# Performance work log

Measured on AMD Instinct MI355X. Metric: run time of the kernel, lower is better.

The kernel has to match this reference:

```python
import jax, jax.numpy as jnp
import numpy as np

B, N, C = 8, 16384, 4
NUM_GROUPS = 512   # K for farthest point sampling
GROUP_SIZE = 32    # K after energy-based top-k
UPSCALE_K = 512    # ball-query candidate count
RADIUS = 0.5       # group_radius
CONTEXT = 256      # context_length


def _fps_idx(xyz, lengths, K):
    """Iterative farthest point sampling. xyz: (B,P,3). Returns (B,K) int32 indices.
    Start point is index 0 (random_start_point=False). Assumes lengths >= K."""
    Bn, P, _ = xyz.shape
    valid = jnp.arange(P)[None, :] < lengths[:, None]
    start = jnp.zeros((Bn,), jnp.int32)
    mind0 = jnp.full((Bn, P), jnp.float32(1e10))

    def step(carry, _):
        mind, last = carry
        lastpt = jnp.take_along_axis(xyz, last[:, None, None], axis=1)  # (B,1,3)
        d = jnp.sum((xyz - lastpt) ** 2, axis=-1)                       # (B,P)
        mind = jnp.minimum(mind, d)
        nxt = jnp.argmax(jnp.where(valid, mind, -jnp.inf), axis=1).astype(jnp.int32)
        return (mind, nxt), nxt

    _, rest = jax.lax.scan(step, (mind0, start), None, length=K - 1)  # (K-1,B)
    return jnp.concatenate([start[:, None], rest.T], axis=1)          # (B,K)


def _masked_gather(points, idx):
    """torch masked_gather: -1 indices are replaced with 0 before gathering."""
    idx0 = jnp.maximum(idx, 0)
    if idx.ndim == 3:
        Bn, G, K = idx.shape
        out = jnp.take_along_axis(points, idx0.reshape(Bn, G * K)[:, :, None], axis=1)
        return out.reshape(Bn, G, K, points.shape[-1])
    return jnp.take_along_axis(points, idx0[:, :, None], axis=1)


def _ball_query(centers, xyz, lengths, K, radius):
    """First-K points within radius of each center, in original index order; pad -1."""
    P = xyz.shape[1]
    d2 = jnp.sum((centers[:, :, None, :] - xyz[:, None, :, :]) ** 2, axis=-1)  # (B,G,P)
    valid = (d2 < radius * radius) & (jnp.arange(P)[None, None, :] < lengths[:, None, None])
    # key = -index for valid points, -P for invalid -> top_k gives first valid indices
    key = jnp.where(valid, -jnp.arange(P, dtype=jnp.int32)[None, None, :], jnp.int32(-P))
    vals, pos = jax.lax.top_k(key, K)           # (B,G,K)
    return jnp.where(vals > -P, pos, -1)


def _topk_by_energy(points, idx, K):
    """Keep the K highest-energy (channel 3) points per group; pad -1."""
    Bn, G, Ko = idx.shape
    e = points[..., 3]                                                  # (B,P)
    eb = jnp.broadcast_to(e[:, None, :], (Bn, G, e.shape[1]))
    energies = jnp.take_along_axis(eb, jnp.maximum(idx, 0), axis=2)     # (B,G,Ko)
    energies = jnp.where(idx == -1, -jnp.inf, energies)
    top_e, top_pos = jax.lax.top_k(energies, K)
    top_idx = jnp.take_along_axis(idx, top_pos, axis=2)
    return jnp.where(jnp.isneginf(top_e), -1, top_idx)


def setup_inputs() -> dict:
    key = jax.random.key(0)
    k1, k2 = jax.random.split(key)
    points = jax.random.normal(k1, (B, N, C), dtype=jnp.float32)
    lengths = jax.random.randint(k2, (B,), 3 * N // 4, N + 1, dtype=jnp.int32)
    return {"points": points, "lengths": lengths}


def reference(points, lengths):
    # FPS -> group centers (kept with all C channels, as in masked_gather(points, idx))
    centers_idx = _fps_idx(points[:, :, :3], lengths, NUM_GROUPS)
    group_centers = _masked_gather(points, centers_idx)                 # (B,G,C)
    # Ball query around centers
    idx = _ball_query(group_centers[:, :, :3], points[:, :, :3], lengths, UPSCALE_K, RADIUS)
    # Energy-based reduction to GROUP_SIZE points per group
    idx = _topk_by_energy(points, idx, GROUP_SIZE)                      # (B,G,Ks)
    point_lengths = jnp.sum(idx != -1, axis=2)                          # (B,G)
    # fill_empty_indices: replace -1 with the group's first index
    filled = jnp.where(idx == -1, idx[:, :, :1], idx)
    groups = _masked_gather(points, filled)                             # (B,G,Ks,C)
    point_mask = jnp.arange(GROUP_SIZE)[None, None, :] < point_lengths[:, :CONTEXT, None]
    G = idx.shape[1]
    group_lengths = jnp.sum(jnp.all(idx != -1, axis=2), axis=1)         # (B,)
    embedding_mask = jnp.arange(G)[None, :] < group_lengths[:, None]
    return (groups[:, :CONTEXT], group_centers[:, :CONTEXT],
            embedding_mask[:, :CONTEXT], point_mask)
```

## Files before the change

kernel.cpp:

```cpp
#include <hip/hip_runtime.h>
#include <stdint.h>

#define NB   8
#define NP   16384
#define NG   512
#define GS   32
#define UPK  512
#define CTX  256

#define OFF_CENTERS (NB*CTX*GS*4)
#define OFF_EMB     (OFF_CENTERS + NB*CTX*4)
#define OFF_PMASK   (OFF_EMB + NB*CTX)

typedef unsigned long long u64;
typedef unsigned int u32;

#define SENT32 0xFFFFFFFFu
#define NWK    31

__device__ __forceinline__ u32 fkey(float f) {
  union { float f; u32 u; } v; v.f = f;
  u32 s = v.u;
  return s ^ ((s & 0x80000000u) ? 0xFFFFFFFFu : 0x80000000u);
}

__device__ __forceinline__ float dist2(float ax, float ay, float az,
                                       float bx, float by, float bz) {
  float dx = __fsub_rn(ax, bx);
  float dy = __fsub_rn(ay, by);
  float dz = __fsub_rn(az, bz);
  return __fadd_rn(__fadd_rn(__fmul_rn(dx, dx), __fmul_rn(dy, dy)),
                   __fmul_rn(dz, dz));
}

template<int CTRL, int RM>
__device__ __forceinline__ u64 dpp_max_u64(u64 k) {
  int lo = (int)(u32)k, hi = (int)(u32)(k >> 32);
  int mlo = __builtin_amdgcn_update_dpp(lo, lo, CTRL, RM, 0xf, false);
  int mhi = __builtin_amdgcn_update_dpp(hi, hi, CTRL, RM, 0xf, false);
  u64 o = ((u64)(u32)mhi << 32) | (u32)mlo;
  return o > k ? o : k;
}

__device__ __forceinline__ u64 wave_max_u64(u64 k) {
  k = dpp_max_u64<0x111, 0xf>(k);
  k = dpp_max_u64<0x112, 0xf>(k);
  k = dpp_max_u64<0x114, 0xf>(k);
  k = dpp_max_u64<0x118, 0xf>(k);
  k = dpp_max_u64<0x142, 0xa>(k);
  k = dpp_max_u64<0x143, 0xc>(k);
  return k;
}

__device__ __forceinline__ u64 read_lane_u64(u64 k, int lane) {
  u32 lo = (u32)__builtin_amdgcn_readlane((int)(u32)k, lane);
  u32 hi = (u32)__builtin_amdgcn_readlane((int)(u32)(k >> 32), lane);
  return ((u64)hi << 32) | lo;
}

struct FpsSmem {
  u64 sred[2][8];
};
struct WkSmem {
  u64 masks[256];
  u32 scnt[256];
  u32 spre[256];
  u32 swsum[8];
  float candE[UPK];
  int   candI[UPK];
  int   s_T, s_pl;
  int   s_fin, s_gl;
  int   s_win[GS];
  float4 s_cc;
};
union SmemU { FpsSmem f; WkSmem w; };
struct Smem { SmemU u; char pad[81920]; };

#define FPS_T 512
#define PPT   (NP / FPS_T)

__global__ __launch_bounds__(FPS_T)
__attribute__((amdgpu_waves_per_eu(2, 2)))
void fused_kernel(const float4* __restrict__ pts, const int* __restrict__ lengths,
                  u32* __restrict__ cws, int* __restrict__ group_len,
                  int* __restrict__ wdone, float* __restrict__ out)
{
  __shared__ Smem sm;
  const int blk  = blockIdx.x;
  const int tid  = threadIdx.x;
  const int lane = tid & 63;
  const int wave = tid >> 6;

  if (blk < NB) {
    FpsSmem& F = sm.u.f;
    const int b = blk;
    const float4* p = pts + (size_t)b * NP;
    const int len = lengths[b];
    u32* cb = cws + (size_t)b * NG;
    if (tid == 0)
      __hip_atomic_store(&cb[0], 0u, __ATOMIC_RELAXED, __HIP_MEMORY_SCOPE_AGENT);

    const float4 q0 = p[0];
    float px[PPT], py[PPT], pz[PPT], mind[PPT];
#pragma unroll
    for (int j = 0; j < PPT; j++) {
      int i = tid + j * FPS_T;
      float4 q = p[i];
      if (i >= len) q = q0;
      px[j] = q.x; py[j] = q.y; pz[j] = q.z;
      mind[j] = 1e10f;
    }

    int last = 0;
    for (int it = 1; it < NG; it++) {
      float4 lp = p[last];
      float tmax = -1.0f; int tj = 0;
#pragma unroll
      for (int j = 0; j < PPT; j++) {
        float d = dist2(px[j], py[j], pz[j], lp.x, lp.y, lp.z);
        float m = fminf(mind[j], d);
        mind[j] = m;
        bool c = m > tmax;
        tmax = c ? m : tmax;
        tj   = c ? j : tj;
      }
      int gidx = tid + (tj << 9);
      u64 key = ((u64)__float_as_uint(tmax) << 32) | (u32)(~gidx);
      key = wave_max_u64(key);
      u64 wkey = read_lane_u64(key, 63);
      if (lane == 0) F.sred[it & 1][wave] = wkey;
      __syncthreads();
      u64 k2 = F.sred[it & 1][lane & 7];
      k2 = dpp_max_u64<0x111, 0xf>(k2);
      k2 = dpp_max_u64<0x112, 0xf>(k2);
      k2 = dpp_max_u64<0x114, 0xf>(k2);
      u64 bk = read_lane_u64(k2, 7);
      last = (int)(~(u32)bk) & (NP - 1);
      if (tid == 0)
        __hip_atomic_store(&cb[it], (u32)last, __ATOMIC_RELAXED,
                           __HIP_MEMORY_SCOPE_AGENT);
    }
    return;
  }

  WkSmem& S = sm.u.w;
  const int b  = blk & (NB - 1);
  const int wi = (blk >> 3) - 1;
  const float4* p = pts + (size_t)b * NP;
  const int len = lengths[b];
  u32* cb = cws + (size_t)b * NG;

  for (int g = wi; g < NG; g += NWK) {
    if (tid == 0) {
      u32 ci;
      while ((ci = __hip_atomic_load(&cb[g], __ATOMIC_RELAXED,
                                     __HIP_MEMORY_SCOPE_AGENT)) == SENT32)
        __builtin_amdgcn_s_sleep(8);
      float4 q = p[ci];
      S.s_cc = q;
      if (g < CTX)
        ((float4*)(out + OFF_CENTERS))[b * CTX + g] = q;
    }
    __syncthreads();
    const float cx = S.s_cc.x, cy = S.s_cc.y, cz = S.s_cc.z;

    if (g >= CTX) {
      u32 c = 0;
      for (int step = 0; step < 32; step++) {
        int i = step * 512 + tid;
        bool flag = false;
        if (i < len) {
          float4 q = p[i];
          float d = dist2(cx, cy, cz, q.x, q.y, q.z);
          flag = d < 0.25f;
        }
        c += (u32)__popcll(__ballot(flag));
        if (c >= GS) break;
      }
      if (lane == 0) S.swsum[wave] = c;
      __syncthreads();
      if (tid == 0) {
        u32 total = 0;
#pragma unroll
        for (int w = 0; w < 8; w++) total += S.swsum[w];
        if (total >= GS) atomicAdd(&group_len[b], 1);
      }
      __syncthreads();
      continue;
    }

    for (int step = 0; step < 32; step++) {
      int i = step * 512 + tid;
      bool flag = false;
      if (i < len) {
        float4 q = p[i];
        float d = dist2(cx, cy, cz, q.x, q.y, q.z);
        flag = d < 0.25f;
      }
      u64 m = __ballot(flag);
      if (lane == 0) S.masks[step * 8 + wave] = m;
    }
    __syncthreads();

    u32 cnt = 0, sc = 0;
    if (tid < 256) {
      cnt = (u32)__popcll(S.masks[tid]);
      sc = cnt;
#pragma unroll
      for (int off = 1; off < 64; off <<= 1) {
        u32 o = __shfl_up(sc, (unsigned)off, 64);
        if (lane >= off) sc += o;
      }
      if (lane == 63) S.swsum[wave] = sc;
    }
    __syncthreads();
    const u32 total = S.swsum[0] + S.swsum[1] + S.swsum[2] + S.swsum[3];
    if (tid < 256) {
      u32 woff = 0;
#pragma unroll
      for (int w = 0; w < 4; w++) woff += (w < wave) ? S.swsum[w] : 0u;
      u32 incl = sc + woff;
      S.scnt[tid] = cnt;
      S.spre[tid] = incl;
      if (total > UPK) {
        u32 ex = incl - cnt;
        if (ex <= (UPK - 1) && incl > (UPK - 1)) {
          u32 r = (UPK - 1) - ex;
          u64 m = S.masks[tid];
          for (u32 k = 0; k < r; k++) m &= m - 1;
          S.s_T = tid * 64 + ((int)__ffsll((unsigned long long)m) - 1);
        }
      } else if (tid == 0) S.s_T = NP - 1;
    }
    __syncthreads();
    const int T = S.s_T;

    for (int step = 0; step < 32; step++) {
      int i  = step * 512 + tid;
      int ch = step * 8 + wave;
      u64 m = S.masks[ch];
      if (((m >> lane) & 1ull) && i <= T) {
        u32 pos = ((S.spre[ch] - S.scnt[ch]) +
                   (u32)__popcll(m & ((1ull << lane) - 1ull))) & (UPK - 1);
        S.candE[pos] = ((const float*)p)[i * 4 + 3];
        S.candI[pos] = i;
      }
    }
    __syncthreads();

    const int ncand = (int)(total < UPK ? total : UPK);

    if (wave == 0) {
      u64 k[8];
#pragma unroll
      for (int t = 0; t < 8; t++) {
        int ci = lane + t * 64;
        k[t] = (ci < ncand) ? (((u64)fkey(S.candE[ci]) << 32) | (u32)(~ci)) : 0ull;
      }
      int pl = 0;
      for (int r = 0; r < GS; r++) {
        u64 bm = k[0];
#pragma unroll
        for (int t = 1; t < 8; t++) if (k[t] > bm) bm = k[t];
#pragma unroll
        for (int off = 32; off; off >>= 1) {
          u64 o = __shfl_xor(bm, (unsigned)off, 64);
          if (o > bm) bm = o;
        }
        if (bm == 0) break;
        int pos = (int)(~(u32)bm) & (UPK - 1);
        if (lane == 0) S.s_win[r] = S.candI[pos];
        int ol = pos & 63, ot = pos >> 6;
#pragma unroll
        for (int t = 0; t < 8; t++)
          if (t == ot && lane == ol) k[t] = 0;
        pl = r + 1;
      }
      if (lane == 0) {
        int f0 = (pl > 0) ? S.s_win[0] : 0;
        for (int r = pl; r < GS; r++) S.s_win[r] = f0;
        S.s_pl = pl;
      }
    }
    __syncthreads();

    const int base = b * CTX + g;
    if (tid < GS) {
      int fi = S.s_win[tid] & (NP - 1);
      float4 q = p[fi];
      ((float4*)out)[base * GS + tid] = q;
      out[OFF_PMASK + base * GS + tid] = (tid < S.s_pl) ? 1.0f : 0.0f;
    }
    if (tid == 0 && total >= GS) atomicAdd(&group_len[b], 1);
    __syncthreads();
  }

  if (tid == 0) {
    int old = __hip_atomic_fetch_add(&wdone[b], 1, __ATOMIC_ACQ_REL,
                                     __HIP_MEMORY_SCOPE_AGENT);
    int fin = (old == NWK - 1) ? 1 : 0;
    S.s_fin = fin;
    S.s_gl = fin ? __hip_atomic_load(&group_len[b], __ATOMIC_RELAXED,
                                     __HIP_MEMORY_SCOPE_AGENT) : 0;
  }
  __syncthreads();
  if (S.s_fin && tid < CTX)
    out[OFF_EMB + b * CTX + tid] = (tid < S.s_gl) ? 1.0f : 0.0f;
}

__global__ void init_kernel(u32* __restrict__ cws, int* __restrict__ group_len,
                            int* __restrict__ wdone)
{
  int i = blockIdx.x * blockDim.x + threadIdx.x;
  if (i < NB * NG)
    __hip_atomic_store(&cws[i], SENT32, __ATOMIC_RELAXED, __HIP_MEMORY_SCOPE_AGENT);
  if (i < NB) { group_len[i] = 0; wdone[i] = 0; }
}

extern "C" void kernel_launch(void* const* d_in, const int* in_sizes, int n_in,
                              void* d_out, int out_size, void* d_ws, size_t ws_size,
                              hipStream_t stream)
{
  const float4* pts     = (const float4*)d_in[0];
  const int*    lengths = (const int*)d_in[1];
  float* out = (float*)d_out;

  u32* cws       = (u32*)d_ws;
  int* group_len = (int*)(cws + NB * NG);
  int* wdone     = group_len + NB;

  init_kernel<<<(NB * NG + 255) / 256, 256, 0, stream>>>(cws, group_len, wdone);
  fused_kernel<<<NB + NB * NWK, FPS_T, 0, stream>>>(pts, lengths, cws, group_len,
                                                    wdone, out);
}
```

Measured before the change: 682.6 us.

## Stage FPS points in LDS and reduce argmax via shared atomicMax slot

The FPS blocks now cache the first 13312 points' xyz in LDS, so the per-iteration fetch of the last selected point usually comes from shared memory instead of global memory. The cross-wave argmax reduction is replaced by a rotating triple-buffered LDS slot updated with a 64-bit atomicMax, which removes the second DPP reduction stage. The per-thread scan now takes the max with v_max3 and recovers the index in a second pass. The 80KB padding array is dropped, which changes LDS use and occupancy for the worker blocks. LDS atomics from eight waves can contend, and the tie-breaking must still pick the same index as before.

```diff
diff --git a/kernel.cpp b/kernel.cpp
--- a/kernel.cpp
+++ b/kernel.cpp
@@ -17,6 +17,7 @@
 
 #define SENT32 0xFFFFFFFFu
 #define NWK    31
+#define NLDS   13312
 
 __device__ __forceinline__ u32 fkey(float f) {
   union { float f; u32 u; } v; v.f = f;
@@ -52,14 +53,9 @@
   return k;
 }
 
-__device__ __forceinline__ u64 read_lane_u64(u64 k, int lane) {
-  u32 lo = (u32)__builtin_amdgcn_readlane((int)(u32)k, lane);
-  u32 hi = (u32)__builtin_amdgcn_readlane((int)(u32)(k >> 32), lane);
-  return ((u64)hi << 32) | lo;
-}
-
 struct FpsSmem {
-  u64 sred[2][8];
+  u64 slot[3];
+  float sx[NLDS], sy[NLDS], sz[NLDS];
 };
 struct WkSmem {
   u64 masks[256];
@@ -74,7 +70,6 @@
   float4 s_cc;
 };
 union SmemU { FpsSmem f; WkSmem w; };
-struct Smem { SmemU u; char pad[81920]; };
 
 #define FPS_T 512
 #define PPT   (NP / FPS_T)
@@ -85,65 +80,81 @@
                   u32* __restrict__ cws, int* __restrict__ group_len,
                   int* __restrict__ wdone, float* __restrict__ out)
 {
-  __shared__ Smem sm;
+  __shared__ SmemU sm;
   const int blk  = blockIdx.x;
   const int tid  = threadIdx.x;
   const int lane = tid & 63;
   const int wave = tid >> 6;
 
   if (blk < NB) {
-    FpsSmem& F = sm.u.f;
+    FpsSmem& F = sm.f;
     const int b = blk;
     const float4* p = pts + (size_t)b * NP;
     const int len = lengths[b];
     u32* cb = cws + (size_t)b * NG;
     if (tid == 0)
       __hip_atomic_store(&cb[0], 0u, __ATOMIC_RELAXED, __HIP_MEMORY_SCOPE_AGENT);
+    if (tid < 3) F.slot[tid] = 0;
 
     const float4 q0 = p[0];
     float px[PPT], py[PPT], pz[PPT], mind[PPT];
 #pragma unroll
     for (int j = 0; j < PPT; j++) {
       int i = tid + j * FPS_T;
-      float4 q = p[i];
+      float4 qr = p[i];
+      if (j < NLDS / FPS_T) {
+        F.sx[i] = qr.x; F.sy[i] = qr.y; F.sz[i] = qr.z;
+      }
+      float4 q = qr;
       if (i >= len) q = q0;
       px[j] = q.x; py[j] = q.y; pz[j] = q.z;
       mind[j] = 1e10f;
     }
+    __syncthreads();
 
     int last = 0;
+    int it3 = 1;
     for (int it = 1; it < NG; it++) {
-      float4 lp = p[last];
-      float tmax = -1.0f; int tj = 0;
+      int ls = __builtin_amdgcn_readfirstlane(last);
+      float lx, ly, lz;
+      if (ls < NLDS) { lx = F.sx[ls]; ly = F.sy[ls]; lz = F.sz[ls]; }
+      else { float4 lp = p[ls]; lx = lp.x; ly = lp.y; lz = lp.z; }
+
 #pragma unroll
       for (int j = 0; j < PPT; j++) {
-        float d = dist2(px[j], py[j], pz[j], lp.x, lp.y, lp.z);
-        float m = fminf(mind[j], d);
-        mind[j] = m;
-        bool c = m > tmax;
-        tmax = c ? m : tmax;
-        tj   = c ? j : tj;
-      }
+        float d = dist2(px[j], py[j], pz[j], lx, ly, lz);
+        mind[j] = fminf(mind[j], d);
+      }
+      float tmax = mind[0];
+#pragma unroll
+      for (int j = 1; j + 1 < PPT; j += 2)
+        asm("v_max3_f32 %0, %0, %1, %2"
+            : "+v"(tmax) : "v"(mind[j]), "v"(mind[j + 1]));
+      tmax = fmaxf(tmax, mind[PPT - 1]);
+      int tj = 0;
+#pragma unroll
+      for (int j = PPT - 1; j >= 0; j--)
+        tj = (mind[j] == tmax) ? j : tj;
+
       int gidx = tid + (tj << 9);
       u64 key = ((u64)__float_as_uint(tmax) << 32) | (u32)(~gidx);
       key = wave_max_u64(key);
-      u64 wkey = read_lane_u64(key, 63);
-      if (lane == 0) F.sred[it & 1][wave] = wkey;
+      if (lane == 63)
+        atomicMax((unsigned long long*)&F.slot[it3], (unsigned long long)key);
+      int iz = it3 + 1; if (iz == 3) iz = 0;
+      if (tid == 0) F.slot[iz] = 0;
       __syncthreads();
-      u64 k2 = F.sred[it & 1][lane & 7];
-      k2 = dpp_max_u64<0x111, 0xf>(k2);
-      k2 = dpp_max_u64<0x112, 0xf>(k2);
-      k2 = dpp_max_u64<0x114, 0xf>(k2);
-      u64 bk = read_lane_u64(k2, 7);
+      u64 bk = F.slot[it3];
       last = (int)(~(u32)bk) & (NP - 1);
       if (tid == 0)
         __hip_atomic_store(&cb[it], (u32)last, __ATOMIC_RELAXED,
                            __HIP_MEMORY_SCOPE_AGENT);
+      it3 = iz;
     }
     return;
   }
 
-  WkSmem& S = sm.u.w;
+  WkSmem& S = sm.w;
   const int b  = blk & (NB - 1);
   const int wi = (blk >> 3) - 1;
   const float4* p = pts + (size_t)b * NP;
```

After: 731.3 us. 7.1% more time.
